# Optimization experiments

Hardware: AMD Instinct MI355X
Metric: run time of the kernel (lower is better)

Reference implementation:

```python
import jax, jax.numpy as jnp
import numpy as np

B, T, D = 1, 4096, 2048
H, HKV = 16, 4
DH = D // H            # 128
GROUP = H // HKV       # 4
ROPE_BASE = 10000.0


def setup_inputs() -> dict:
    key = jax.random.key(0)
    kx, kq, kk, kv, ko = jax.random.split(key, 5)
    s = 0.02
    return {
        "x": jax.random.normal(kx, (B, T, D), dtype=jnp.float32),
        "Wq": jax.random.normal(kq, (D, D), dtype=jnp.float32) * s,
        "Wk": jax.random.normal(kk, (D, HKV * DH), dtype=jnp.float32) * s,
        "Wv": jax.random.normal(kv, (D, HKV * DH), dtype=jnp.float32) * s,
        "Wo": jax.random.normal(ko, (D, D), dtype=jnp.float32) * s,
    }


def _rope_sincos(t, half):
    inv_freq = 1.0 / (ROPE_BASE ** (jnp.arange(half, dtype=jnp.float32) / half))
    ang = jnp.arange(t, dtype=jnp.float32)[:, None] * inv_freq  # [T, half]
    # broadcast over batch and head dims: [1, T, 1, half]
    return jnp.sin(ang)[None, :, None, :], jnp.cos(ang)[None, :, None, :]


def _apply_rope(x, sin, cos, half):
    x1, x2 = x[..., :half], x[..., half:]
    return jnp.concatenate([x1 * cos - x2 * sin, x1 * sin + x2 * cos], axis=-1)


def reference(x, Wq, Wk, Wv, Wo):
    b, t, d = x.shape
    q = (x @ Wq).reshape(b, t, H, DH)      # [B,T,H,Dh], H ordered (Hkv, group)
    k = (x @ Wk).reshape(b, t, HKV, DH)    # [B,T,Hkv,Dh]
    v = (x @ Wv).reshape(b, t, HKV, DH)

    half = DH // 2
    sin, cos = _rope_sincos(t, half)
    q = _apply_rope(q, sin, cos, half)
    k = _apply_rope(k, sin, cos, half)

    # GQA without materializing repeated K/V: split q heads into (kv_head, group)
    qg = q.reshape(b, t, HKV, GROUP, DH)
    att = jnp.einsum('bthgd,bshd->bhgts', qg, k) / np.float32(np.sqrt(DH))
    causal = jnp.tril(jnp.ones((t, t), dtype=bool))
    att = jnp.where(causal[None, None, None, :, :], att, -jnp.inf)
    att = jax.nn.softmax(att, axis=-1)
    y = jnp.einsum('bhgts,bshd->bthgd', att, v).reshape(b, t, d)
    return y @ Wo
```

## Files before the change

### kernel.cpp

```cpp
#include <hip/hip_runtime.h>
#include <hip/hip_bf16.h>

#define TT 4096
#define DD 2048
#define NH 16
#define NKV 4
#define DHD 128
#define NQKV 3072

typedef __attribute__((ext_vector_type(8))) short short8;
typedef __attribute__((ext_vector_type(4))) float f32x4;
typedef __hip_bfloat16 bf16;

#define GLOAD_LDS16(g, l)                                                \
    __builtin_amdgcn_global_load_lds(                                    \
        (const __attribute__((address_space(1))) unsigned int*)(g),      \
        (__attribute__((address_space(3))) unsigned int*)(l), 16, 0, 0)

__global__ void cast_x_kernel(const float* __restrict__ x, bf16* __restrict__ xb, int n) {
    int i = (blockIdx.x * blockDim.x + threadIdx.x) * 4;
    if (i >= n) return;
    float4 v = *(const float4*)(x + i);
    xb[i + 0] = __float2bfloat16(v.x);
    xb[i + 1] = __float2bfloat16(v.y);
    xb[i + 2] = __float2bfloat16(v.z);
    xb[i + 3] = __float2bfloat16(v.w);
}

__global__ void transpose_cast_all(const float* __restrict__ Wq, const float* __restrict__ Wk,
                                   const float* __restrict__ Wv, const float* __restrict__ Wo,
                                   bf16* __restrict__ Wt, bf16* __restrict__ Wot) {
    __shared__ float tile[32][33];
    const float* in;
    bf16* out;
    int N, rowOff;
    switch (blockIdx.z) {
        case 0: in = Wq; out = Wt; N = 2048; rowOff = 0; break;
        case 1: in = Wk; out = Wt; N = 512; rowOff = 2048; break;
        case 2: in = Wv; out = Wt; N = 512; rowOff = 2560; break;
        default: in = Wo; out = Wot; N = 2048; rowOff = 0; break;
    }
    int n0 = blockIdx.y * 32;
    if (n0 >= N) return;
    int k0 = blockIdx.x * 32;
    int tx = threadIdx.x, ty = threadIdx.y;
#pragma unroll
    for (int i = 0; i < 4; ++i)
        tile[ty + i * 8][tx] = in[(size_t)(k0 + ty + i * 8) * N + n0 + tx];
    __syncthreads();
#pragma unroll
    for (int i = 0; i < 4; ++i)
        out[(size_t)(rowOff + n0 + ty + i * 8) * 2048 + k0 + tx] = __float2bfloat16(tile[tx][ty + i * 8]);
}

template <bool OUT_BF16>
__global__ __launch_bounds__(256) void gemm_bt_kernel(const bf16* __restrict__ A,
                                                      const bf16* __restrict__ Bt,
                                                      void* __restrict__ C,
                                                      int M, int N, int K) {
    __shared__ bf16 As[128 * 32];
    __shared__ bf16 Bs[128 * 32];
    int nwg = gridDim.x * gridDim.y;
    int orig = blockIdx.y * gridDim.x + blockIdx.x;
    int swz = (orig & 7) * (nwg >> 3) + (orig >> 3);
    int bx = swz % gridDim.x, by = swz / gridDim.x;
    int bn0 = bx * 128, bm0 = by * 128;
    int tid = threadIdx.x;
    int wave = tid >> 6, lane = tid & 63, quad = lane >> 4, l15 = lane & 15;
    int wm = (wave >> 1) * 64, wn = (wave & 1) * 64;

    int srow = wave * 32 + (lane >> 2);
    int scol = (lane & 3) * 8;
    const bf16* gA = A + (size_t)(bm0 + srow) * K + scol;
    const bf16* gB = Bt + (size_t)(bn0 + srow) * K + scol;
    bf16* lA = As + srow * 32 + scol;
    bf16* lB = Bs + srow * 32 + scol;

    f32x4 zero = {0.f, 0.f, 0.f, 0.f};
    f32x4 acc[4][4];
#pragma unroll
    for (int i = 0; i < 4; ++i)
#pragma unroll
        for (int j = 0; j < 4; ++j) acc[i][j] = zero;

    for (int k0 = 0; k0 < K; k0 += 32) {
        GLOAD_LDS16(gA + k0, lA);
        GLOAD_LDS16(gA + k0 + (size_t)16 * K, lA + 16 * 32);
        GLOAD_LDS16(gB + k0, lB);
        GLOAD_LDS16(gB + k0 + (size_t)16 * K, lB + 16 * 32);
        __syncthreads();
        short8 af[4], bfr[4];
#pragma unroll
        for (int i = 0; i < 4; ++i) af[i] = *(const short8*)&As[(wm + i * 16 + l15) * 32 + quad * 8];
#pragma unroll
        for (int j = 0; j < 4; ++j) bfr[j] = *(const short8*)&Bs[(wn + j * 16 + l15) * 32 + quad * 8];
#pragma unroll
        for (int i = 0; i < 4; ++i)
#pragma unroll
            for (int j = 0; j < 4; ++j)
                acc[i][j] = __builtin_amdgcn_mfma_f32_16x16x32_bf16(af[i], bfr[j], acc[i][j], 0, 0, 0);
        __syncthreads();
    }
#pragma unroll
    for (int i = 0; i < 4; ++i)
#pragma unroll
        for (int j = 0; j < 4; ++j)
#pragma unroll
            for (int r = 0; r < 4; ++r) {
                int row = bm0 + wm + i * 16 + quad * 4 + r;
                int col = bn0 + wn + j * 16 + l15;
                float v = acc[i][j][r];
                if (OUT_BF16)
                    ((bf16*)C)[(size_t)row * N + col] = __float2bfloat16(v);
                else
                    ((float*)C)[(size_t)row * N + col] = v;
            }
}

__global__ void rope_split_kernel(const bf16* __restrict__ QKV, bf16* __restrict__ Qs,
                                  bf16* __restrict__ Ks, bf16* __restrict__ Vr) {
    int slot = blockIdx.x * 4 + (threadIdx.x >> 6);
    int d = threadIdx.x & 63;
    int t = slot / 24, c = slot % 24;
    const bf16* base = QKV + (size_t)t * NQKV;
    int off = (c < 16) ? c * 128 : (c < 20) ? 2048 + (c - 16) * 128 : 2560 + (c - 20) * 128;
    float x1 = __bfloat162float(base[off + d]);
    float x2 = __bfloat162float(base[off + 64 + d]);
    float o1, o2;
    if (c < 20) {
        float invf = __expf((float)d * -0.14391156831f);
        float ang = (float)t * invf;
        float sn = sinf(ang), cs = cosf(ang);
        o1 = x1 * cs - x2 * sn;
        o2 = x1 * sn + x2 * cs;
    } else {
        o1 = x1;
        o2 = x2;
    }
    if (c < 16) {
        const float scale = 0.12751741f;
        o1 *= scale;
        o2 *= scale;
        bf16* dst = Qs + ((size_t)c * TT + t) * DHD;
        dst[d] = __float2bfloat16(o1);
        dst[d + 64] = __float2bfloat16(o2);
    } else if (c < 20) {
        bf16* dst = Ks + ((size_t)(c - 16) * TT + t) * DHD;
        dst[d] = __float2bfloat16(o1);
        dst[d + 64] = __float2bfloat16(o2);
    } else {
        int gg = c - 20;
        bf16* dst = Vr + ((size_t)gg * TT + t) * DHD;
        dst[d] = __float2bfloat16(o1);
        dst[d + 64] = __float2bfloat16(o2);
    }
}

__global__ void transpose_v_kernel(const bf16* __restrict__ Vr, bf16* __restrict__ Vt) {
    __shared__ short tile[64][80];
    int g = blockIdx.z;
    int t0 = blockIdx.x * 64, d0 = blockIdx.y * 64;
    int tid = threadIdx.x;
#pragma unroll
    for (int i = 0; i < 2; ++i) {
        int lin = i * 2048 + tid * 8;
        int r = lin >> 6, c = lin & 63;
        *(short8*)&tile[r][c] = *(const short8*)(Vr + ((size_t)g * TT + t0 + r) * DHD + d0 + c);
    }
    __syncthreads();
#pragma unroll
    for (int i = 0; i < 2; ++i) {
        int lin = i * 2048 + tid * 8;
        int r = lin >> 6, c = lin & 63;
        short8 v;
#pragma unroll
        for (int j = 0; j < 8; ++j) v[j] = tile[c + j][r];
        *(short8*)(Vt + ((size_t)g * DHD + d0 + r) * TT + t0 + c) = v;
    }
}

__global__ __launch_bounds__(512, 4) void attn_kernel(const bf16* __restrict__ Qs,
                                                      const bf16* __restrict__ Ks,
                                                      const bf16* __restrict__ Vt,
                                                      bf16* __restrict__ Y) {
    __shared__ __attribute__((aligned(16))) char smem[74752];
    int h = blockIdx.y, bpair = blockIdx.x, g = h >> 2;
    int tid = threadIdx.x, wave = tid >> 6, lane = tid & 63, quad = lane >> 4, l15 = lane & 15;
    int grp = wave >> 2;
    int w = wave & 3;
    int gtid = tid & 255;

    char* Kbase = smem + grp * 32768;
    bf16* PsW = (bf16*)(smem + 65536 + wave * 1024);
    float* Obuf = (float*)(smem + 32768);
    float* mlbuf = (float*)(smem + 73728);

    const bf16* kg = Ks + (size_t)g * TT * DHD;
    const bf16* vg = Vt + (size_t)g * DHD * TT;
    f32x4 zero = {0.f, 0.f, 0.f, 0.f};

    int kOff[2], vOff[2], lOff[2];
#pragma unroll
    for (int r = 0; r < 2; ++r) {
        int idx = r * 256 + gtid;
        int krow = idx >> 4;
        kOff[r] = krow * DHD + ((idx & 15) ^ (krow & 15)) * 8;
        int vrow = idx >> 2;
        vOff[r] = vrow * TT + ((idx & 3) ^ ((vrow >> 1) & 3)) * 8;
        lOff[r] = idx * 8;
    }
    int fsw = (l15 >> 1) & 3;

    for (int pass = 0; pass < 2; ++pass) {
        int qt = (pass == 0) ? bpair : 63 - bpair;
        int qbase = qt * 64 + w * 16;

        short8 qf[4];
        const bf16* qptr = Qs + ((size_t)h * TT + qbase + l15) * DHD + quad * 8;
#pragma unroll
        for (int ks = 0; ks < 4; ++ks) qf[ks] = *(const short8*)(qptr + ks * 32);

        f32x4 acc[8];
#pragma unroll
        for (int i = 0; i < 8; ++i) acc[i] = zero;
        float m_i = -1e30f, l_i = 0.f;

        const bf16* kS = kg + (size_t)(grp * 32) * DHD;
        const bf16* vS = vg + grp * 32;
        int nIter = qt + 1;

#pragma unroll
        for (int r = 0; r < 2; ++r) {
            GLOAD_LDS16(kS + kOff[r], (bf16*)Kbase + lOff[r]);
            GLOAD_LDS16(vS + vOff[r], (bf16*)(Kbase + 16384) + lOff[r]);
        }
        __syncthreads();

        int boff = 0;
        for (int j = 0; j < nIter; ++j) {
            int kt = 2 * j + grp;
            if (j + 1 < nIter) {
#pragma unroll
                for (int r = 0; r < 2; ++r) {
                    GLOAD_LDS16(kS + 64 * DHD + kOff[r], (bf16*)(Kbase + (boff ^ 8192)) + lOff[r]);
                    GLOAD_LDS16(vS + 64 + vOff[r], (bf16*)(Kbase + 16384 + (boff ^ 8192)) + lOff[r]);
                }
            }
            const bf16* Kl = (const bf16*)(Kbase + boff);
            const bf16* Vl = (const bf16*)(Kbase + 16384 + boff);
            int dbase = 2 * kt - 4 * qt - w;
            if (dbase <= 0) {
                f32x4 s[2];
                __builtin_amdgcn_s_setprio(1);
#pragma unroll
                for (int nt = 0; nt < 2; ++nt) {
                    int dnt = dbase + nt;
                    if (dnt <= 0) {
                        s[nt] = zero;
#pragma unroll
                        for (int ks = 0; ks < 4; ++ks) {
                            int ch = (ks * 4 + quad) ^ l15;
                            short8 kf = *(const short8*)&Kl[(nt * 16 + l15) * 128 + ch * 8];
                            s[nt] = __builtin_amdgcn_mfma_f32_16x16x32_bf16(kf, qf[ks], s[nt], 0, 0, 0);
                        }
                        if (dnt == 0) {
#pragma unroll
                            for (int r = 0; r < 4; ++r)
                                if (quad * 4 + r > l15) s[nt][r] = -1e30f;
                        }
                    } else {
#pragma unroll
                        for (int r = 0; r < 4; ++r) s[nt][r] = -1e30f;
                    }
                }
                __builtin_amdgcn_s_setprio(0);

                float mloc = -1e30f;
#pragma unroll
                for (int nt = 0; nt < 2; ++nt)
#pragma unroll
                    for (int r = 0; r < 4; ++r) mloc = fmaxf(mloc, s[nt][r]);
                mloc = fmaxf(mloc, __shfl_xor(mloc, 16));
                mloc = fmaxf(mloc, __shfl_xor(mloc, 32));
                float mnew = fmaxf(m_i, mloc);
                bool up = __any(mloc > m_i);
                float alpha = up ? exp2f(m_i - mnew) : 1.0f;
                float sl = 0.f;
#pragma unroll
                for (int nt = 0; nt < 2; ++nt)
#pragma unroll
                    for (int r = 0; r < 4; ++r) {
                        s[nt][r] = exp2f(s[nt][r] - mnew);
                        sl += s[nt][r];
                    }
                sl += __shfl_xor(sl, 16);
                sl += __shfl_xor(sl, 32);
                l_i = l_i * alpha + sl;
                m_i = mnew;
                if (up) {
#pragma unroll
                    for (int d8 = 0; d8 < 8; ++d8)
#pragma unroll
                        for (int r = 0; r < 4; ++r) acc[d8][r] *= alpha;
                }

#pragma unroll
                for (int nt = 0; nt < 2; ++nt)
#pragma unroll
                    for (int rr = 0; rr < 2; ++rr) {
                        int col = nt * 16 + quad * 4 + rr * 2;
                        int ch = (col >> 3) ^ fsw;
                        __hip_bfloat162 pk;
                        pk.x = __float2bfloat16(s[nt][rr * 2]);
                        pk.y = __float2bfloat16(s[nt][rr * 2 + 1]);
                        *(__hip_bfloat162*)&PsW[l15 * 32 + ch * 8 + (col & 7)] = pk;
                    }
                asm volatile("s_waitcnt lgkmcnt(0)" ::: "memory");

                int chp = quad ^ fsw;
                short8 pf = *(const short8*)&PsW[l15 * 32 + chp * 8];
                __builtin_amdgcn_s_setprio(1);
#pragma unroll
                for (int d8 = 0; d8 < 8; ++d8) {
                    short8 vf = *(const short8*)&Vl[(d8 * 16 + l15) * 32 + chp * 8];
                    acc[d8] = __builtin_amdgcn_mfma_f32_16x16x32_bf16(vf, pf, acc[d8], 0, 0, 0);
                }
                __builtin_amdgcn_s_setprio(0);
            }
            __syncthreads();
            boff ^= 8192;
            kS += 64 * DHD;
            vS += 64;
        }

        if (quad == 0) {
            mlbuf[(wave * 16 + l15) * 2] = m_i;
            mlbuf[(wave * 16 + l15) * 2 + 1] = l_i;
        }
        __syncthreads();
        if (grp == 1) {
            float m_a = mlbuf[(w * 16 + l15) * 2];
            float mm = fmaxf(m_a, m_i);
            float fb = exp2f(m_i - mm);
            float* ob = Obuf + (w * 16 + l15) * 132;
#pragma unroll
            for (int d8 = 0; d8 < 8; ++d8) {
                f32x4 t = acc[d8] * fb;
                *(f32x4*)&ob[d8 * 16 + quad * 4] = t;
            }
        }
        __syncthreads();
        if (grp == 0) {
            float m_b = mlbuf[((w + 4) * 16 + l15) * 2];
            float l_b = mlbuf[((w + 4) * 16 + l15) * 2 + 1];
            float mm = fmaxf(m_i, m_b);
            float fa = exp2f(m_i - mm);
            float fb = exp2f(m_b - mm);
            float lt = l_i * fa + l_b * fb;
            float* ob = Obuf + (w * 16 + l15) * 132;
#pragma unroll
            for (int d8 = 0; d8 < 8; ++d8) {
                f32x4 t = *(const f32x4*)&ob[d8 * 16 + quad * 4];
                acc[d8] = acc[d8] * fa + t;
            }
            float linv = 1.0f / lt;

            bf16* ow = (bf16*)smem + w * 2048;
#pragma unroll
            for (int d8 = 0; d8 < 8; ++d8)
#pragma unroll
                for (int rr = 0; rr < 2; ++rr) {
                    int colD = d8 * 16 + quad * 4 + rr * 2;
                    int ch = (colD >> 3) ^ (l15 & 7);
                    __hip_bfloat162 o2;
                    o2.x = __float2bfloat16(acc[d8][rr * 2] * linv);
                    o2.y = __float2bfloat16(acc[d8][rr * 2 + 1] * linv);
                    *(__hip_bfloat162*)&ow[l15 * 128 + ch * 8 + (colD & 7)] = o2;
                }
            asm volatile("s_waitcnt lgkmcnt(0)" ::: "memory");
#pragma unroll
            for (int c = 0; c < 4; ++c) {
                int chunk = quad * 4 + c;
                int ch = chunk ^ (l15 & 7);
                short8 ov = *(const short8*)&ow[l15 * 128 + ch * 8];
                *(short8*)&Y[(size_t)(qbase + l15) * DD + h * DHD + chunk * 8] = ov;
            }
        }
        __syncthreads();
    }
}

extern "C" void kernel_launch(void* const* d_in, const int* in_sizes, int n_in,
                              void* d_out, int out_size, void* d_ws, size_t ws_size,
                              hipStream_t stream) {
    const float* x = (const float*)d_in[0];
    const float* Wq = (const float*)d_in[1];
    const float* Wk = (const float*)d_in[2];
    const float* Wv = (const float*)d_in[3];
    const float* Wo = (const float*)d_in[4];

    char* ws = (char*)d_ws;
    size_t off = 0;
    auto alloc = [&](size_t bytes) {
        void* p = ws + off;
        off += (bytes + 255) & ~(size_t)255;
        return p;
    };
    bf16* xb = (bf16*)alloc((size_t)TT * DD * 2);
    bf16* Wt = (bf16*)alloc((size_t)NQKV * DD * 2);
    bf16* Wot = (bf16*)alloc((size_t)DD * DD * 2);
    bf16* QKVb = (bf16*)alloc((size_t)TT * NQKV * 2);
    bf16* Qs = (bf16*)alloc((size_t)NH * TT * DHD * 2);
    bf16* Ksb = (bf16*)alloc((size_t)NKV * TT * DHD * 2);
    bf16* Vrb = (bf16*)alloc((size_t)NKV * TT * DHD * 2);
    bf16* Vtb = (bf16*)alloc((size_t)NKV * DHD * TT * 2);
    bf16* Yb = (bf16*)alloc((size_t)TT * DD * 2);

    cast_x_kernel<<<(TT * DD / 4 + 255) / 256, 256, 0, stream>>>(x, xb, TT * DD);
    transpose_cast_all<<<dim3(64, 64, 4), dim3(32, 8), 0, stream>>>(Wq, Wk, Wv, Wo, Wt, Wot);

    gemm_bt_kernel<true><<<dim3(NQKV / 128, TT / 128), 256, 0, stream>>>(xb, Wt, QKVb, TT, NQKV, DD);
    rope_split_kernel<<<TT * 24 / 4, 256, 0, stream>>>(QKVb, Qs, Ksb, Vrb);
    transpose_v_kernel<<<dim3(TT / 64, DHD / 64, NKV), 256, 0, stream>>>(Vrb, Vtb);
    attn_kernel<<<dim3(32, NH), 512, 0, stream>>>(Qs, Ksb, Vtb, Yb);
    gemm_bt_kernel<false><<<dim3(DD / 128, TT / 128), 256, 0, stream>>>(Yb, Wot, d_out, TT, DD, DD);
}
```

Baseline: 394.9 us.

## Fold softmax row-sum into PV MFMA via ones row and lazy rescaling

Appends a constant ones row to each V tile in shared memory so that one extra MFMA accumulates the softmax denominator, which removes the per-iteration exp-sum and cross-lane shuffles. It also switches to lazy max rescaling that only rescales when the running max grows by more than 8 (log2 units). The change enlarges shared memory and reshuffles buffer offsets, and the final row sum is now read back from the extra accumulator. The trade is one more MFMA and more LDS per iteration against fewer VALU and shuffle operations, and larger exponent ranges, which remain bounded by the threshold.

Measured after the change: 396.9 us. Within noise of the previous version (+0.5%).

```diff
diff --git a/kernel.cpp b/kernel.cpp
--- a/kernel.cpp
+++ b/kernel.cpp
@@ -183,17 +183,17 @@
                                                       const bf16* __restrict__ Ks,
                                                       const bf16* __restrict__ Vt,
                                                       bf16* __restrict__ Y) {
-    __shared__ __attribute__((aligned(16))) char smem[74752];
+    __shared__ __attribute__((aligned(16))) char smem[78848];
     int h = blockIdx.y, bpair = blockIdx.x, g = h >> 2;
     int tid = threadIdx.x, wave = tid >> 6, lane = tid & 63, quad = lane >> 4, l15 = lane & 15;
     int grp = wave >> 2;
     int w = wave & 3;
     int gtid = tid & 255;
 
-    char* Kbase = smem + grp * 32768;
-    bf16* PsW = (bf16*)(smem + 65536 + wave * 1024);
-    float* Obuf = (float*)(smem + 32768);
-    float* mlbuf = (float*)(smem + 73728);
+    char* Kbase = smem + grp * 34816;
+    bf16* PsW = (bf16*)(smem + 69632 + wave * 1024);
+    float* Obuf = (float*)(smem + 16384);
+    float* mlbuf = (float*)(smem + 77824);
 
     const bf16* kg = Ks + (size_t)g * TT * DHD;
     const bf16* vg = Vt + (size_t)g * DHD * TT;
@@ -215,15 +215,22 @@
         int qt = (pass == 0) ? bpair : 63 - bpair;
         int qbase = qt * 64 + w * 16;
 
+        if (tid < 256) {
+            int g2 = tid >> 7, b2 = (tid >> 6) & 1, e0 = (tid & 63) * 8;
+            short fill = (e0 < 32) ? (short)0x3F80 : (short)0;
+            short8 v8 = {fill, fill, fill, fill, fill, fill, fill, fill};
+            *(short8*)((bf16*)(smem + g2 * 34816 + 16384 + b2 * 9216) + 4096 + e0) = v8;
+        }
+
         short8 qf[4];
         const bf16* qptr = Qs + ((size_t)h * TT + qbase + l15) * DHD + quad * 8;
 #pragma unroll
         for (int ks = 0; ks < 4; ++ks) qf[ks] = *(const short8*)(qptr + ks * 32);
 
-        f32x4 acc[8];
-#pragma unroll
-        for (int i = 0; i < 8; ++i) acc[i] = zero;
-        float m_i = -1e30f, l_i = 0.f;
+        f32x4 acc[9];
+#pragma unroll
+        for (int i = 0; i < 9; ++i) acc[i] = zero;
+        float m_i = -1e30f;
 
         const bf16* kS = kg + (size_t)(grp * 32) * DHD;
         const bf16* vS = vg + grp * 32;
@@ -236,18 +243,18 @@
         }
         __syncthreads();
 
-        int boff = 0;
+        int jb = 0;
         for (int j = 0; j < nIter; ++j) {
             int kt = 2 * j + grp;
             if (j + 1 < nIter) {
 #pragma unroll
                 for (int r = 0; r < 2; ++r) {
-                    GLOAD_LDS16(kS + 64 * DHD + kOff[r], (bf16*)(Kbase + (boff ^ 8192)) + lOff[r]);
-                    GLOAD_LDS16(vS + 64 + vOff[r], (bf16*)(Kbase + 16384 + (boff ^ 8192)) + lOff[r]);
+                    GLOAD_LDS16(kS + 64 * DHD + kOff[r], (bf16*)(Kbase + (jb ? 0 : 8192)) + lOff[r]);
+                    GLOAD_LDS16(vS + 64 + vOff[r], (bf16*)(Kbase + 16384 + (jb ? 0 : 9216)) + lOff[r]);
                 }
             }
-            const bf16* Kl = (const bf16*)(Kbase + boff);
-            const bf16* Vl = (const bf16*)(Kbase + 16384 + boff);
+            const bf16* Kl = (const bf16*)(Kbase + (jb ? 8192 : 0));
+            const bf16* Vl = (const bf16*)(Kbase + 16384 + (jb ? 9216 : 0));
             int dbase = 2 * kt - 4 * qt - w;
             if (dbase <= 0) {
                 f32x4 s[2];
@@ -275,34 +282,23 @@
                 }
                 __builtin_amdgcn_s_setprio(0);
 
-                float mloc = -1e30f;
-#pragma unroll
-                for (int nt = 0; nt < 2; ++nt)
-#pragma unroll
-                    for (int r = 0; r < 4; ++r) mloc = fmaxf(mloc, s[nt][r]);
+                float mloc = fmaxf(fmaxf(s[0][0], s[0][1]), fmaxf(s[0][2], s[0][3]));
+                mloc = fmaxf(mloc, fmaxf(fmaxf(s[1][0], s[1][1]), fmaxf(s[1][2], s[1][3])));
                 mloc = fmaxf(mloc, __shfl_xor(mloc, 16));
                 mloc = fmaxf(mloc, __shfl_xor(mloc, 32));
-                float mnew = fmaxf(m_i, mloc);
-                bool up = __any(mloc > m_i);
-                float alpha = up ? exp2f(m_i - mnew) : 1.0f;
-                float sl = 0.f;
-#pragma unroll
-                for (int nt = 0; nt < 2; ++nt)
-#pragma unroll
-                    for (int r = 0; r < 4; ++r) {
-                        s[nt][r] = exp2f(s[nt][r] - mnew);
-                        sl += s[nt][r];
-                    }
-                sl += __shfl_xor(sl, 16);
-                sl += __shfl_xor(sl, 32);
-                l_i = l_i * alpha + sl;
-                m_i = mnew;
-                if (up) {
-#pragma unroll
-                    for (int d8 = 0; d8 < 8; ++d8)
+                if (__any(mloc > m_i + 8.0f)) {
+                    float mnew = fmaxf(m_i, mloc);
+                    float alpha = exp2f(m_i - mnew);
+                    m_i = mnew;
+#pragma unroll
+                    for (int d8 = 0; d8 < 9; ++d8)
 #pragma unroll
                         for (int r = 0; r < 4; ++r) acc[d8][r] *= alpha;
                 }
+#pragma unroll
+                for (int nt = 0; nt < 2; ++nt)
+#pragma unroll
+                    for (int r = 0; r < 4; ++r) s[nt][r] = exp2f(s[nt][r] - m_i);
 
 #pragma unroll
                 for (int nt = 0; nt < 2; ++nt)
@@ -321,21 +317,21 @@
                 short8 pf = *(const short8*)&PsW[l15 * 32 + chp * 8];
                 __builtin_amdgcn_s_setprio(1);
 #pragma unroll
-                for (int d8 = 0; d8 < 8; ++d8) {
+                for (int d8 = 0; d8 < 9; ++d8) {
                     short8 vf = *(const short8*)&Vl[(d8 * 16 + l15) * 32 + chp * 8];
                     acc[d8] = __builtin_amdgcn_mfma_f32_16x16x32_bf16(vf, pf, acc[d8], 0, 0, 0);
                 }
                 __builtin_amdgcn_s_setprio(0);
             }
             __syncthreads();
-            boff ^= 8192;
+            jb ^= 1;
             kS += 64 * DHD;
             vS += 64;
         }
 
         if (quad == 0) {
             mlbuf[(wave * 16 + l15) * 2] = m_i;
-            mlbuf[(wave * 16 + l15) * 2 + 1] = l_i;
+            mlbuf[(wave * 16 + l15) * 2 + 1] = acc[8][0];
         }
         __syncthreads();
         if (grp == 1) {
@@ -353,10 +349,11 @@
         if (grp == 0) {
             float m_b = mlbuf[((w + 4) * 16 + l15) * 2];
             float l_b = mlbuf[((w + 4) * 16 + l15) * 2 + 1];
+            float l_a = mlbuf[(w * 16 + l15) * 2 + 1];
             float mm = fmaxf(m_i, m_b);
             float fa = exp2f(m_i - mm);
             float fb = exp2f(m_b - mm);
-            float lt = l_i * fa + l_b * fb;
+            float lt = l_a * fa + l_b * fb;
             float* ob = Obuf + (w * 16 + l15) * 132;
 #pragma unroll
             for (int d8 = 0; d8 < 8; ++d8) {
```
